# Kernel tuning notes

Measured on AMD Instinct MI355X. Metric: run time of the kernel, lower is better.

## Reference

```python
import jax, jax.numpy as jnp
import numpy as np

# ---- module hyperparameters (from init_kwargs) ----
K_CURV = 1.0      # Lorentz curvature k
MAX_NORM = 1000.0 # rescale_to_max cap on space-norm (assumed)
KSIZE = 5
STRIDE = 2
PAD = 2
IN_CH = 257       # includes time dim -> 256 space channels
OUT_CH = 257
LIN_FEATS = (IN_CH - 1) * KSIZE + 1  # 1281
EPS = 1e-8


def _add_time(space):
    # time = sqrt(k + ||space||^2), concat on last axis
    time = jnp.sqrt(K_CURV + jnp.sum(space * space, axis=-1, keepdims=True))
    return jnp.concatenate([time, space], axis=-1)


def _rescale_to_max(x):
    # clamp space-norm to MAX_NORM, then recompute valid time component
    space = x[..., 1:]
    norm = jnp.sqrt(jnp.sum(space * space, axis=-1, keepdims=True))
    scale = jnp.minimum(1.0, MAX_NORM / jnp.maximum(norm, EPS))
    return _add_time(space * scale)


def setup_inputs() -> dict:
    key = jax.random.key(0)
    kx, kw, kb = jax.random.split(key, 3)
    x = jax.random.normal(kx, (16, 8192, IN_CH), dtype=jnp.float32)
    W = jax.random.normal(kw, (OUT_CH, LIN_FEATS), dtype=jnp.float32) * 0.02
    b = jax.random.normal(kb, (OUT_CH,), dtype=jnp.float32) * 0.01
    return {"x": x, "W": W, "b": b}


def reference(x, W, b):
    B, L, C = x.shape
    # pad length dim with zeros (time channel of padded frames is clamped in
    # torch, but the time channel is discarded before add_time, so only the
    # space channels matter)
    xp = jnp.pad(x, ((0, 0), (PAD, PAD), (0, 0)))
    space = xp[..., 1:]                                  # (B, Lp, C-1)
    Lp = L + 2 * PAD
    n_frames = (Lp - KSIZE) // STRIDE + 1
    # im2col gather: (n_frames, K) window indices
    idx = jnp.arange(n_frames)[:, None] * STRIDE + jnp.arange(KSIZE)[None, :]
    patches = space[:, idx, :]                           # (B, n, K, C-1)
    # torch reorders to kernel-major (k, c) layout before add_time
    ps = patches.reshape(B, n_frames, KSIZE * (C - 1))   # (B, n, K*(C-1))
    pk = _add_time(ps)                                   # (B, n, lin_feats)
    out = jnp.einsum('bnf,of->bno', pk, W) + b           # LorentzProjection
    out = _add_time(out[..., 1:])                        # manifold.projx
    out = _rescale_to_max(out)                           # rescale_after=True
    return out
```

## Files before the change

### kernel.cpp

```cpp
#include <hip/hip_runtime.h>
#include <hip/hip_bf16.h>
#include <cstdint>
#include <cstddef>

namespace {

constexpr int BATCH = 16;
constexpr int LEN   = 8192;
constexpr int CIN   = 257;
constexpr int CS    = 256;
constexpr int NF    = 4096;
constexpr int KG    = 1280;
constexpr int MT    = 128;
constexpr int NITER = 20;

constexpr size_t WT_BYTES = (size_t)CS * KG * 2;
constexpr size_t W0_OFF   = WT_BYTES;
constexpr size_t WS_NEED  = W0_OFF + (size_t)CS * 4;

typedef __attribute__((ext_vector_type(8))) short short8;
typedef __attribute__((ext_vector_type(8))) unsigned short ushort8v;
typedef __attribute__((ext_vector_type(4))) float f32x4;

__device__ __forceinline__ unsigned short f2bf_bits(float f) {
  union { __hip_bfloat16 h; unsigned short u; } cv;
  cv.h = __float2bfloat16(f);
  return cv.u;
}

__device__ __forceinline__ void async_cp16(const void* g, void* l) {
  __builtin_amdgcn_global_load_lds(
      (const __attribute__((address_space(1))) void*)g,
      (__attribute__((address_space(3))) void*)l,
      16, 0, 0);
}

}

__global__ void prep_w_kernel(const float* __restrict__ W,
                              __hip_bfloat16* __restrict__ wt,
                              float* __restrict__ w0) {
  int n = blockIdx.x;
  const float* wrow = W + (size_t)(n + 1) * 1281;
  for (int k = threadIdx.x; k < KG; k += blockDim.x)
    wt[(size_t)n * KG + k] = __float2bfloat16(wrow[1 + k]);
  if (threadIdx.x == 0) w0[n] = wrow[0];
}

__global__ __launch_bounds__(512, 2) void lorentz_fused_kernel(
    const float* __restrict__ x,
    const __hip_bfloat16* __restrict__ wt,
    const float* __restrict__ w0,
    const float* __restrict__ bvec,
    float* __restrict__ out) {
  __shared__ alignas(16) char lds[98304];
  __shared__ alignas(16) float time0_s[128];
  __shared__ alignas(16) float normsq_s[128];
  char* const A0 = lds;
  char* const A1 = lds + 16384;
  char* const B0 = lds + 32768;
  char* const B1 = lds + 65536;

  const int tid   = threadIdx.x;
  const int w     = tid >> 6;
  const int lane  = tid & 63;
  const int row16 = lane & 15;
  const int q     = lane >> 4;
  const int mh    = w >> 2;
  const int nq    = w & 3;
  const int lg    = lane >> 3;
  const int lc    = lane & 7;
  const int csw   = lc ^ lg;

  const int bx    = blockIdx.x;
  const int b     = bx >> 5;
  const int Mblk  = (bx & 31) * MT;

  const int m0 = w * 16 + lg;
  const int m1 = m0 + 8;
  const float* xb = x + (size_t)b * LEN * CIN;

  f32x4 acc[4][4];
#pragma unroll
  for (int i = 0; i < 4; ++i)
#pragma unroll
    for (int j = 0; j < 4; ++j) acc[i][j] = (f32x4){0.f, 0.f, 0.f, 0.f};

  float ssq0 = 0.f, ssq1 = 0.f;
  f32x4 a00, a01, a10, a11;

  auto loadA = [&](int it) {
    const int kk = it >> 2;
    const int c0 = (it & 3) << 6;
    const int coff = 1 + c0 + lc * 8;
    const int t0 = 2 * (Mblk + m0) + kk - 2;
    const int t1 = t0 + 16;
    a00 = (f32x4){0.f, 0.f, 0.f, 0.f};
    a01 = a00; a10 = a00; a11 = a00;
    if ((unsigned)t0 < (unsigned)LEN) {
      const float* g = xb + (size_t)t0 * CIN + coff;
      __builtin_memcpy(&a00, g, 16);
      __builtin_memcpy(&a01, g + 4, 16);
    }
    if ((unsigned)t1 < (unsigned)LEN) {
      const float* g = xb + (size_t)t1 * CIN + coff;
      __builtin_memcpy(&a10, g, 16);
      __builtin_memcpy(&a11, g + 4, 16);
    }
  };

  auto writeA = [&](char* A) {
    ssq0 += a00[0]*a00[0] + a00[1]*a00[1] + a00[2]*a00[2] + a00[3]*a00[3]
          + a01[0]*a01[0] + a01[1]*a01[1] + a01[2]*a01[2] + a01[3]*a01[3];
    ssq1 += a10[0]*a10[0] + a10[1]*a10[1] + a10[2]*a10[2] + a10[3]*a10[3]
          + a11[0]*a11[0] + a11[1]*a11[1] + a11[2]*a11[2] + a11[3]*a11[3];
    ushort8v u0, u1;
#pragma unroll
    for (int i = 0; i < 4; ++i) {
      u0[i]     = f2bf_bits(a00[i]);
      u0[4 + i] = f2bf_bits(a01[i]);
      u1[i]     = f2bf_bits(a10[i]);
      u1[4 + i] = f2bf_bits(a11[i]);
    }
    *(ushort8v*)(A + ((m0 * 8 + csw) << 4)) = u0;
    *(ushort8v*)(A + ((m1 * 8 + csw) << 4)) = u1;
  };

  auto stageB = [&](int it, char* B) {
    const int k0 = it << 6;
#pragma unroll
    for (int j = 0; j < 4; ++j) {
      const int n = w * 32 + j * 8 + lg;
      async_cp16(wt + (size_t)n * KG + k0 + csw * 8, B + (w * 4 + j) * 1024);
    }
  };

  auto compute = [&](const char* A, const char* B) {
#pragma unroll
    for (int s = 0; s < 2; ++s) {
      const int p = (s * 4 + q) ^ lc;
      short8 bfr[4];
#pragma unroll
      for (int nt = 0; nt < 4; ++nt)
        bfr[nt] = *(const short8*)(B + (((nq * 64 + nt * 16 + row16) * 8 + p) << 4));
#pragma unroll
      for (int mt = 0; mt < 4; ++mt) {
        short8 af = *(const short8*)(A + (((mh * 64 + mt * 16 + row16) * 8 + p) << 4));
#pragma unroll
        for (int nt = 0; nt < 4; ++nt)
          acc[mt][nt] = __builtin_amdgcn_mfma_f32_16x16x32_bf16(
              af, bfr[nt], acc[mt][nt], 0, 0, 0);
      }
    }
  };

  loadA(0);
  stageB(0, B0);
  asm volatile("s_waitcnt vmcnt(4)" ::: "memory");
  writeA(A0);
  loadA(1);
  asm volatile("s_waitcnt lgkmcnt(0)" ::: "memory");

  for (int it = 0; it < NITER; ++it) {
    char* Ac = (it & 1) ? A1 : A0;
    char* Bc = (it & 1) ? B1 : B0;
    if (it < NITER - 1) {
      char* An = (it & 1) ? A0 : A1;
      char* Bn = (it & 1) ? B0 : B1;
      stageB(it + 1, Bn);
      asm volatile("s_waitcnt vmcnt(4)" ::: "memory");
      writeA(An);
      if (it < NITER - 2) loadA(it + 2);
    } else {
      asm volatile("s_waitcnt vmcnt(0)" ::: "memory");
    }
    asm volatile("" ::: "memory");
    __builtin_amdgcn_s_barrier();
    asm volatile("" ::: "memory");
    compute(Ac, Bc);
    asm volatile("" ::: "memory");
    __builtin_amdgcn_s_barrier();
    asm volatile("" ::: "memory");
  }

  if (tid < 128) normsq_s[tid] = 0.0f;
  {
    float s0 = ssq0;
    s0 += __shfl_xor(s0, 1); s0 += __shfl_xor(s0, 2); s0 += __shfl_xor(s0, 4);
    float s1 = ssq1;
    s1 += __shfl_xor(s1, 1); s1 += __shfl_xor(s1, 2); s1 += __shfl_xor(s1, 4);
    if (lc == 0) {
      time0_s[m0] = sqrtf(1.0f + s0);
      time0_s[m1] = sqrtf(1.0f + s1);
    }
  }
  __syncthreads();

  float w0v[4], bv[4];
#pragma unroll
  for (int nt = 0; nt < 4; ++nt) {
    int n = nq * 64 + nt * 16 + row16;
    w0v[nt] = w0[n];
    bv[nt]  = bvec[1 + n];
  }

#pragma unroll
  for (int mt = 0; mt < 4; ++mt) {
    f32x4 t4 = *(const f32x4*)&time0_s[mh * 64 + mt * 16 + q * 4];
#pragma unroll
    for (int nt = 0; nt < 4; ++nt)
#pragma unroll
      for (int r = 0; r < 4; ++r)
        acc[mt][nt][r] = acc[mt][nt][r] + t4[r] * w0v[nt] + bv[nt];
#pragma unroll
    for (int r = 0; r < 4; ++r) {
      float ps = 0.f;
#pragma unroll
      for (int nt = 0; nt < 4; ++nt) ps += acc[mt][nt][r] * acc[mt][nt][r];
      ps += __shfl_xor(ps, 1);
      ps += __shfl_xor(ps, 2);
      ps += __shfl_xor(ps, 4);
      ps += __shfl_xor(ps, 8);
      if (row16 == 0) atomicAdd(&normsq_s[mh * 64 + mt * 16 + q * 4 + r], ps);
    }
  }
  __syncthreads();

#pragma unroll
  for (int mt = 0; mt < 4; ++mt) {
#pragma unroll
    for (int r = 0; r < 4; ++r) {
      int m = mh * 64 + mt * 16 + q * 4 + r;
      float nsq  = normsq_s[m];
      float norm = sqrtf(nsq);
      float scale = fminf(1.0f, 1000.0f / fmaxf(norm, 1e-8f));
      size_t ob = ((size_t)b * NF + Mblk + m) * 257;
#pragma unroll
      for (int nt = 0; nt < 4; ++nt) {
        int n = nq * 64 + nt * 16 + row16;
        out[ob + 1 + n] = acc[mt][nt][r] * scale;
      }
    }
  }
  if (tid < 128) {
    float nsq  = normsq_s[tid];
    float norm = sqrtf(nsq);
    float scale = fminf(1.0f, 1000.0f / fmaxf(norm, 1e-8f));
    size_t ob = ((size_t)b * NF + Mblk + tid) * 257;
    out[ob] = sqrtf(1.0f + scale * scale * nsq);
  }
}

__global__ void fallback_kernel(const float* __restrict__ x,
                                const float* __restrict__ W,
                                const float* __restrict__ bvec,
                                float* __restrict__ out) {
  int fid = blockIdx.x;
  int b = fid >> 12;
  int g = fid & (NF - 1);
  __shared__ float patch[1280];
  __shared__ float red[256];
  int tid = threadIdx.x;
  float ss = 0.f;
  for (int k = tid; k < 1280; k += 256) {
    int kk = k >> 8, c = k & 255;
    int t = 2 * g + kk - 2;
    float v = (t >= 0 && t < LEN) ? x[((size_t)b * LEN + t) * CIN + 1 + c] : 0.f;
    patch[k] = v;
    ss += v * v;
  }
  red[tid] = ss;
  __syncthreads();
  for (int off = 128; off > 0; off >>= 1) {
    if (tid < off) red[tid] += red[tid + off];
    __syncthreads();
  }
  float time0 = sqrtf(1.f + red[0]);
  __syncthreads();
  const float* wrow = W + (size_t)(tid + 1) * 1281;
  float acc = time0 * wrow[0] + bvec[tid + 1];
  for (int k = 0; k < 1280; ++k) acc += wrow[1 + k] * patch[k];
  red[tid] = acc * acc;
  __syncthreads();
  for (int off = 128; off > 0; off >>= 1) {
    if (tid < off) red[tid] += red[tid + off];
    __syncthreads();
  }
  float nsq = red[0];
  float norm = sqrtf(nsq);
  float scale = fminf(1.f, 1000.f / fmaxf(norm, 1e-8f));
  size_t ob = ((size_t)b * NF + g) * 257;
  out[ob + 1 + tid] = acc * scale;
  if (tid == 0) out[ob] = sqrtf(1.f + scale * scale * nsq);
}

extern "C" void kernel_launch(void* const* d_in, const int* in_sizes, int n_in,
                              void* d_out, int out_size, void* d_ws, size_t ws_size,
                              hipStream_t stream) {
  const float* x  = (const float*)d_in[0];
  const float* W  = (const float*)d_in[1];
  const float* bv = (const float*)d_in[2];
  float* out = (float*)d_out;

  if (ws_size >= WS_NEED) {
    char* ws = (char*)d_ws;
    __hip_bfloat16* wt = (__hip_bfloat16*)ws;
    float* w0          = (float*)(ws + W0_OFF);
    prep_w_kernel<<<256, 256, 0, stream>>>(W, wt, w0);
    lorentz_fused_kernel<<<BATCH * (NF / MT), 512, 0, stream>>>(x, wt, w0, bv, out);
  } else {
    fallback_kernel<<<BATCH * NF, 256, 0, stream>>>(x, W, bv, out);
  }
}
```

Measured before the change: 268.8 us.

## Replace double-buffered LDS pipeline with single buffer to halve shared memory

Drops the ping-pong A/B LDS buffers in favour of one 48KB buffer set. Each iteration now writes A, issues the async B copy, prefetches the next A tile and then computes, with two full __syncthreads per iteration. The aim is to let two 512-thread blocks reside per CU instead of one, so the 512-block grid can run in a single wave. The cost is the in-block overlap of loads with MFMA compute: the barriers likely force outstanding global loads to drain before compute.

```diff
diff --git a/kernel.cpp b/kernel.cpp
--- a/kernel.cpp
+++ b/kernel.cpp
@@ -53,13 +53,10 @@
     const float* __restrict__ w0,
     const float* __restrict__ bvec,
     float* __restrict__ out) {
-  __shared__ alignas(16) char lds[98304];
+  __shared__ alignas(16) char A_lds[16384];
+  __shared__ alignas(16) char B_lds[32768];
   __shared__ alignas(16) float time0_s[128];
   __shared__ alignas(16) float normsq_s[128];
-  char* const A0 = lds;
-  char* const A1 = lds + 16384;
-  char* const B0 = lds + 32768;
-  char* const B1 = lds + 65536;
 
   const int tid   = threadIdx.x;
   const int w     = tid >> 6;
@@ -109,7 +106,7 @@
     }
   };
 
-  auto writeA = [&](char* A) {
+  auto writeA = [&]() {
     ssq0 += a00[0]*a00[0] + a00[1]*a00[1] + a00[2]*a00[2] + a00[3]*a00[3]
           + a01[0]*a01[0] + a01[1]*a01[1] + a01[2]*a01[2] + a01[3]*a01[3];
     ssq1 += a10[0]*a10[0] + a10[1]*a10[1] + a10[2]*a10[2] + a10[3]*a10[3]
@@ -122,30 +119,30 @@
       u1[i]     = f2bf_bits(a10[i]);
       u1[4 + i] = f2bf_bits(a11[i]);
     }
-    *(ushort8v*)(A + ((m0 * 8 + csw) << 4)) = u0;
-    *(ushort8v*)(A + ((m1 * 8 + csw) << 4)) = u1;
-  };
-
-  auto stageB = [&](int it, char* B) {
+    *(ushort8v*)(A_lds + ((m0 * 8 + csw) << 4)) = u0;
+    *(ushort8v*)(A_lds + ((m1 * 8 + csw) << 4)) = u1;
+  };
+
+  auto stageB = [&](int it) {
     const int k0 = it << 6;
 #pragma unroll
     for (int j = 0; j < 4; ++j) {
       const int n = w * 32 + j * 8 + lg;
-      async_cp16(wt + (size_t)n * KG + k0 + csw * 8, B + (w * 4 + j) * 1024);
-    }
-  };
-
-  auto compute = [&](const char* A, const char* B) {
+      async_cp16(wt + (size_t)n * KG + k0 + csw * 8, B_lds + (w * 4 + j) * 1024);
+    }
+  };
+
+  auto compute = [&]() {
 #pragma unroll
     for (int s = 0; s < 2; ++s) {
       const int p = (s * 4 + q) ^ lc;
       short8 bfr[4];
 #pragma unroll
       for (int nt = 0; nt < 4; ++nt)
-        bfr[nt] = *(const short8*)(B + (((nq * 64 + nt * 16 + row16) * 8 + p) << 4));
+        bfr[nt] = *(const short8*)(B_lds + (((nq * 64 + nt * 16 + row16) * 8 + p) << 4));
 #pragma unroll
       for (int mt = 0; mt < 4; ++mt) {
-        short8 af = *(const short8*)(A + (((mh * 64 + mt * 16 + row16) * 8 + p) << 4));
+        short8 af = *(const short8*)(A_lds + (((mh * 64 + mt * 16 + row16) * 8 + p) << 4));
 #pragma unroll
         for (int nt = 0; nt < 4; ++nt)
           acc[mt][nt] = __builtin_amdgcn_mfma_f32_16x16x32_bf16(
@@ -155,34 +152,16 @@
   };
 
   loadA(0);
-  stageB(0, B0);
-  asm volatile("s_waitcnt vmcnt(4)" ::: "memory");
-  writeA(A0);
-  loadA(1);
-  asm volatile("s_waitcnt lgkmcnt(0)" ::: "memory");
-
   for (int it = 0; it < NITER; ++it) {
-    char* Ac = (it & 1) ? A1 : A0;
-    char* Bc = (it & 1) ? B1 : B0;
-    if (it < NITER - 1) {
-      char* An = (it & 1) ? A0 : A1;
-      char* Bn = (it & 1) ? B0 : B1;
-      stageB(it + 1, Bn);
-      asm volatile("s_waitcnt vmcnt(4)" ::: "memory");
-      writeA(An);
-      if (it < NITER - 2) loadA(it + 2);
-    } else {
-      asm volatile("s_waitcnt vmcnt(0)" ::: "memory");
-    }
-    asm volatile("" ::: "memory");
-    __builtin_amdgcn_s_barrier();
-    asm volatile("" ::: "memory");
-    compute(Ac, Bc);
-    asm volatile("" ::: "memory");
-    __builtin_amdgcn_s_barrier();
-    asm volatile("" ::: "memory");
-  }
-
+    __syncthreads();
+    writeA();
+    stageB(it);
+    if (it + 1 < NITER) loadA(it + 1);
+    __syncthreads();
+    compute();
+  }
+
+  __syncthreads();
   if (tid < 128) normsq_s[tid] = 0.0f;
   {
     float s0 = ssq0;
```

Result: slower. 285.5 us (+6.2%).

## Triple-buffer B tiles and overlap A staging with split MFMA phases

Applied to the files above, without the earlier changes.

Restructures the main loop into a deeper software pipeline. B tiles go into three LDS buffers and are prefetched two iterations ahead. A tiles use two alternating register sets, and the bf16 conversion and LDS write of the next A tile sit between the two k-halves of the MFMA work. The loop now needs one barrier per iteration instead of two, and s_setprio raises wave priority around the MFMA bursts. The cost is more LDS (an extra 32 KB B buffer), more live registers, and vmcnt bookkeeping that depends on the exact count of outstanding loads.

```diff
diff --git a/kernel.cpp b/kernel.cpp
--- a/kernel.cpp
+++ b/kernel.cpp
@@ -22,6 +22,8 @@
 typedef __attribute__((ext_vector_type(8))) unsigned short ushort8v;
 typedef __attribute__((ext_vector_type(4))) float f32x4;
 
+struct ARegs { f32x4 a00, a01, a10, a11; };
+
 __device__ __forceinline__ unsigned short f2bf_bits(float f) {
   union { __hip_bfloat16 h; unsigned short u; } cv;
   cv.h = __float2bfloat16(f);
@@ -53,13 +55,10 @@
     const float* __restrict__ w0,
     const float* __restrict__ bvec,
     float* __restrict__ out) {
-  __shared__ alignas(16) char lds[98304];
+  __shared__ alignas(16) char Ab[2][16384];
+  __shared__ alignas(16) char Bb[3][32768];
   __shared__ alignas(16) float time0_s[128];
   __shared__ alignas(16) float normsq_s[128];
-  char* const A0 = lds;
-  char* const A1 = lds + 16384;
-  char* const B0 = lds + 32768;
-  char* const B1 = lds + 65536;
 
   const int tid   = threadIdx.x;
   const int w     = tid >> 6;
@@ -86,41 +85,41 @@
 #pragma unroll
     for (int j = 0; j < 4; ++j) acc[i][j] = (f32x4){0.f, 0.f, 0.f, 0.f};
 
+  ARegs afE, afO;
   float ssq0 = 0.f, ssq1 = 0.f;
-  f32x4 a00, a01, a10, a11;
-
-  auto loadA = [&](int it) {
+
+  auto loadA = [&](int it, ARegs& af) {
     const int kk = it >> 2;
     const int c0 = (it & 3) << 6;
     const int coff = 1 + c0 + lc * 8;
     const int t0 = 2 * (Mblk + m0) + kk - 2;
     const int t1 = t0 + 16;
-    a00 = (f32x4){0.f, 0.f, 0.f, 0.f};
-    a01 = a00; a10 = a00; a11 = a00;
+    af.a00 = (f32x4){0.f, 0.f, 0.f, 0.f};
+    af.a01 = af.a00; af.a10 = af.a00; af.a11 = af.a00;
     if ((unsigned)t0 < (unsigned)LEN) {
       const float* g = xb + (size_t)t0 * CIN + coff;
-      __builtin_memcpy(&a00, g, 16);
-      __builtin_memcpy(&a01, g + 4, 16);
+      __builtin_memcpy(&af.a00, g, 16);
+      __builtin_memcpy(&af.a01, g + 4, 16);
     }
     if ((unsigned)t1 < (unsigned)LEN) {
       const float* g = xb + (size_t)t1 * CIN + coff;
-      __builtin_memcpy(&a10, g, 16);
-      __builtin_memcpy(&a11, g + 4, 16);
-    }
-  };
-
-  auto writeA = [&](char* A) {
-    ssq0 += a00[0]*a00[0] + a00[1]*a00[1] + a00[2]*a00[2] + a00[3]*a00[3]
-          + a01[0]*a01[0] + a01[1]*a01[1] + a01[2]*a01[2] + a01[3]*a01[3];
-    ssq1 += a10[0]*a10[0] + a10[1]*a10[1] + a10[2]*a10[2] + a10[3]*a10[3]
-          + a11[0]*a11[0] + a11[1]*a11[1] + a11[2]*a11[2] + a11[3]*a11[3];
+      __builtin_memcpy(&af.a10, g, 16);
+      __builtin_memcpy(&af.a11, g + 4, 16);
+    }
+  };
+
+  auto writeA = [&](char* A, ARegs& af) {
+    ssq0 += af.a00[0]*af.a00[0] + af.a00[1]*af.a00[1] + af.a00[2]*af.a00[2] + af.a00[3]*af.a00[3]
+          + af.a01[0]*af.a01[0] + af.a01[1]*af.a01[1] + af.a01[2]*af.a01[2] + af.a01[3]*af.a01[3];
+    ssq1 += af.a10[0]*af.a10[0] + af.a10[1]*af.a10[1] + af.a10[2]*af.a10[2] + af.a10[3]*af.a10[3]
+          + af.a11[0]*af.a11[0] + af.a11[1]*af.a11[1] + af.a11[2]*af.a11[2] + af.a11[3]*af.a11[3];
     ushort8v u0, u1;
 #pragma unroll
     for (int i = 0; i < 4; ++i) {
-      u0[i]     = f2bf_bits(a00[i]);
-      u0[4 + i] = f2bf_bits(a01[i]);
-      u1[i]     = f2bf_bits(a10[i]);
-      u1[4 + i] = f2bf_bits(a11[i]);
+      u0[i]     = f2bf_bits(af.a00[i]);
+      u0[4 + i] = f2bf_bits(af.a01[i]);
+      u1[i]     = f2bf_bits(af.a10[i]);
+      u1[4 + i] = f2bf_bits(af.a11[i]);
     }
     *(ushort8v*)(A + ((m0 * 8 + csw) << 4)) = u0;
     *(ushort8v*)(A + ((m1 * 8 + csw) << 4)) = u1;
@@ -135,54 +134,63 @@
     }
   };
 
-  auto compute = [&](const char* A, const char* B) {
-#pragma unroll
-    for (int s = 0; s < 2; ++s) {
-      const int p = (s * 4 + q) ^ lc;
-      short8 bfr[4];
+  auto mfma_s = [&](const char* A, const char* B, int s) {
+    const int p = (s * 4 + q) ^ lc;
+    short8 bfr[4];
+#pragma unroll
+    for (int nt = 0; nt < 4; ++nt)
+      bfr[nt] = *(const short8*)(B + (((nq * 64 + nt * 16 + row16) * 8 + p) << 4));
+    __builtin_amdgcn_s_setprio(1);
+#pragma unroll
+    for (int mt = 0; mt < 4; ++mt) {
+      short8 af = *(const short8*)(A + (((mh * 64 + mt * 16 + row16) * 8 + p) << 4));
 #pragma unroll
       for (int nt = 0; nt < 4; ++nt)
-        bfr[nt] = *(const short8*)(B + (((nq * 64 + nt * 16 + row16) * 8 + p) << 4));
-#pragma unroll
-      for (int mt = 0; mt < 4; ++mt) {
-        short8 af = *(const short8*)(A + (((mh * 64 + mt * 16 + row16) * 8 + p) << 4));
-#pragma unroll
-        for (int nt = 0; nt < 4; ++nt)
-          acc[mt][nt] = __builtin_amdgcn_mfma_f32_16x16x32_bf16(
-              af, bfr[nt], acc[mt][nt], 0, 0, 0);
-      }
-    }
-  };
-
-  loadA(0);
-  stageB(0, B0);
-  asm volatile("s_waitcnt vmcnt(4)" ::: "memory");
-  writeA(A0);
-  loadA(1);
+        acc[mt][nt] = __builtin_amdgcn_mfma_f32_16x16x32_bf16(
+            af, bfr[nt], acc[mt][nt], 0, 0, 0);
+    }
+    __builtin_amdgcn_s_setprio(0);
+  };
+
+  stageB(0, Bb[0]);
+  loadA(0, afE);
+  asm volatile("s_waitcnt vmcnt(0)" ::: "memory");
+  writeA(Ab[0], afE);
+  loadA(1, afO);
+  stageB(1, Bb[1]);
   asm volatile("s_waitcnt lgkmcnt(0)" ::: "memory");
-
-  for (int it = 0; it < NITER; ++it) {
-    char* Ac = (it & 1) ? A1 : A0;
-    char* Bc = (it & 1) ? B1 : B0;
-    if (it < NITER - 1) {
-      char* An = (it & 1) ? A0 : A1;
-      char* Bn = (it & 1) ? B0 : B1;
-      stageB(it + 1, Bn);
+  asm volatile("" ::: "memory");
+  __builtin_amdgcn_s_barrier();
+  asm volatile("" ::: "memory");
+
+  auto iterBody = [&](int it, ARegs& regsC, ARegs& regsF) {
+    char* Acur = Ab[it & 1];
+    char* Anxt = Ab[(it + 1) & 1];
+    char* Bcur = Bb[it % 3];
+    if (it + 2 < NITER) stageB(it + 2, Bb[(it + 2) % 3]);
+    mfma_s(Acur, Bcur, 0);
+    if (it + 2 < NITER) {
       asm volatile("s_waitcnt vmcnt(4)" ::: "memory");
-      writeA(An);
-      if (it < NITER - 2) loadA(it + 2);
-    } else {
+    } else if (it + 1 < NITER) {
       asm volatile("s_waitcnt vmcnt(0)" ::: "memory");
     }
-    asm volatile("" ::: "memory");
-    __builtin_amdgcn_s_barrier();
-    asm volatile("" ::: "memory");
-    compute(Ac, Bc);
-    asm volatile("" ::: "memory");
-    __builtin_amdgcn_s_barrier();
-    asm volatile("" ::: "memory");
-  }
-
+    if (it + 1 < NITER) writeA(Anxt, regsC);
+    if (it + 2 < NITER) loadA(it + 2, regsF);
+    mfma_s(Acur, Bcur, 1);
+    if (it + 1 < NITER) {
+      asm volatile("s_waitcnt lgkmcnt(0)" ::: "memory");
+      asm volatile("" ::: "memory");
+      __builtin_amdgcn_s_barrier();
+      asm volatile("" ::: "memory");
+    }
+  };
+
+  for (int it = 0; it < NITER; it += 2) {
+    iterBody(it,     afO, afE);
+    iterBody(it + 1, afE, afO);
+  }
+
+  __syncthreads();
   if (tid < 128) normsq_s[tid] = 0.0f;
   {
     float s0 = ssq0;
```

Result: slower. 277.1 us (+3.1%).

## Pre-convert x to padded bf16 and use 256-row GEMM tiles with async loads

Applied to the files above, without the earlier changes.

Adds a prep pass that converts x to a padded bf16 buffer and precomputes per-row squared norms. A new GEMM kernel then streams A and B tiles straight into LDS with async global-to-LDS copies, uses 256x256 output tiles with triple-buffered B, and raises MFMA priority. The intent is to halve the activation bytes the GEMM reads and to cut per-block conversion and reduction work, at the cost of an extra full pass over x and a large workspace. With 160KB of LDS per block, occupancy drops to one block per CU.

```diff
diff --git a/kernel.cpp b/kernel.cpp
--- a/kernel.cpp
+++ b/kernel.cpp
@@ -11,12 +11,18 @@
 constexpr int CS    = 256;
 constexpr int NF    = 4096;
 constexpr int KG    = 1280;
-constexpr int MT    = 128;
 constexpr int NITER = 20;
-
-constexpr size_t WT_BYTES = (size_t)CS * KG * 2;
-constexpr size_t W0_OFF   = WT_BYTES;
-constexpr size_t WS_NEED  = W0_OFF + (size_t)CS * 4;
+constexpr int LPAD  = LEN + 4;
+
+constexpr size_t XS_BYTES  = (size_t)BATCH * LPAD * CS * 2;
+constexpr size_t RSQ_OFF   = XS_BYTES;
+constexpr size_t RSQ_BYTES = (size_t)BATCH * LPAD * 4;
+constexpr size_t WT1_OFF   = RSQ_OFF + RSQ_BYTES;
+constexpr size_t W01_OFF   = WT1_OFF + (size_t)CS * KG * 2;
+constexpr size_t WS1_NEED  = W01_OFF + (size_t)CS * 4;
+
+constexpr size_t W02_OFF  = (size_t)CS * KG * 2;
+constexpr size_t WS2_NEED = W02_OFF + (size_t)CS * 4;
 
 typedef __attribute__((ext_vector_type(8))) short short8;
 typedef __attribute__((ext_vector_type(8))) unsigned short ushort8v;
@@ -47,19 +53,254 @@
   if (threadIdx.x == 0) w0[n] = wrow[0];
 }
 
+__global__ void prep_x_kernel(const float* __restrict__ x,
+                              __hip_bfloat16* __restrict__ xs,
+                              float* __restrict__ rowsq) {
+  const int tid = threadIdx.x;
+  const int bx  = blockIdx.x;
+  if (bx < 8192) {
+    __shared__ float4 xf4[1028];
+    const float4* src = (const float4*)(x + (size_t)bx * 4112);
+#pragma unroll
+    for (int i = 0; i < 4; ++i) {
+      int idx = i * 256 + tid;
+      xf4[idx] = src[idx];
+    }
+    if (tid < 4) xf4[1024 + tid] = src[1024 + tid];
+    __syncthreads();
+    const float* xf = (const float*)xf4;
+    const int row = tid >> 4, seg = tid & 15;
+    const float* v = xf + row * 257 + 1 + seg * 16;
+    float ss = 0.f;
+    unsigned short u[16];
+#pragma unroll
+    for (int i = 0; i < 16; ++i) {
+      float f = v[i];
+      ss += f * f;
+      u[i] = f2bf_bits(f);
+    }
+    const int b = bx >> 9;
+    const int t = (bx & 511) * 16 + row;
+    const size_t tpg = (size_t)b * LPAD + 2 + t;
+    ushort8v* dst = (ushort8v*)((unsigned short*)xs + tpg * CS + seg * 16);
+    ushort8v p0, p1;
+#pragma unroll
+    for (int i = 0; i < 8; ++i) { p0[i] = u[i]; p1[i] = u[8 + i]; }
+    dst[0] = p0;
+    dst[1] = p1;
+    ss += __shfl_xor(ss, 1);
+    ss += __shfl_xor(ss, 2);
+    ss += __shfl_xor(ss, 4);
+    ss += __shfl_xor(ss, 8);
+    if (seg == 0) rowsq[tpg] = ss;
+  } else {
+    for (int i = tid; i < 64 * 128; i += 256) {
+      int row = i >> 7, uo = i & 127;
+      int b = row >> 2, j = row & 3;
+      size_t tpg = (size_t)b * LPAD + (j < 2 ? j : 8192 + j);
+      ((uint32_t*)xs)[tpg * 128 + uo] = 0;
+      if (uo == 0) rowsq[tpg] = 0.0f;
+    }
+  }
+}
+
+__global__ __launch_bounds__(512, 2) void lorentz_gemm8_kernel(
+    const __hip_bfloat16* __restrict__ xs,
+    const __hip_bfloat16* __restrict__ wt,
+    const float* __restrict__ rowsq,
+    const float* __restrict__ w0,
+    const float* __restrict__ bvec,
+    float* __restrict__ out) {
+  __shared__ alignas(16) char lds[163840];
+
+  const int tid   = threadIdx.x;
+  const int w     = tid >> 6;
+  const int lane  = tid & 63;
+  const int row16 = lane & 15;
+  const int q     = lane >> 4;
+  const int wr    = w >> 2;
+  const int wc    = w & 3;
+  const int lg    = lane >> 3;
+  const int lc    = lane & 7;
+  const int csw   = lc ^ lg;
+
+  const int bx    = blockIdx.x;
+  const int b     = bx >> 4;
+  const int Mblk  = (bx & 15) * 256;
+
+  const __hip_bfloat16* xsb = xs + (size_t)b * LPAD * CS;
+
+  f32x4 acc[8][4];
+#pragma unroll
+  for (int i = 0; i < 8; ++i)
+#pragma unroll
+    for (int j = 0; j < 4; ++j) acc[i][j] = (f32x4){0.f, 0.f, 0.f, 0.f};
+
+  auto stgA = [&](int t, int hf, char* buf) {
+    char* dst = buf + hf * 16384 + w * 2048;
+#pragma unroll
+    for (int j = 0; j < 2; ++j) {
+      const int r  = w * 16 + j * 8 + lg;
+      const int rp = 2 * (Mblk + hf * 128 + r) + (t >> 2);
+      async_cp16(xsb + (size_t)rp * CS + ((t & 3) << 6) + csw * 8,
+                 dst + j * 1024);
+    }
+  };
+  auto stgB = [&](int t, int hf, char* buf) {
+    char* dst = buf + hf * 16384 + w * 2048;
+#pragma unroll
+    for (int j = 0; j < 2; ++j) {
+      const int n = hf * 128 + w * 16 + j * 8 + lg;
+      async_cp16(wt + (size_t)n * KG + (t << 6) + csw * 8, dst + j * 1024);
+    }
+  };
+
+  auto rdA = [&](const char* Ah, int mt, int s) -> short8 {
+    const int lr = mt * 16 + row16;
+    const int p  = (s * 4 + q) ^ lc;
+    return *(const short8*)(Ah + ((lr * 8 + p) << 4));
+  };
+  auto rdB = [&](const char* Bh, int nt, int s) -> short8 {
+    const int lr = (wc & 1) * 64 + nt * 16 + row16;
+    const int p  = (s * 4 + q) ^ lc;
+    return *(const short8*)(Bh + ((lr * 8 + p) << 4));
+  };
+
+  char* Acur = lds;
+  char* Aalt = lds + 32768;
+  char* Bcur = lds + 65536;
+  char* Bnx  = lds + 65536 + 32768;
+  char* Bnn  = lds + 65536 + 65536;
+
+  stgB(0, 0, Bcur); stgB(0, 1, Bcur);
+  stgA(0, 0, Acur); stgA(0, 1, Acur);
+  stgB(1, 0, Bnx);  stgB(1, 1, Bnx);
+  asm volatile("s_waitcnt vmcnt(4)" ::: "memory");
+  asm volatile("" ::: "memory");
+  __builtin_amdgcn_s_barrier();
+  asm volatile("" ::: "memory");
+
+  for (int t = 0; t < NITER; ++t) {
+    const char* Ah = Acur + (wr << 14);
+    const char* Bh = Bcur + ((wc >> 1) << 14);
+    short8 bfr[4];
+#pragma unroll
+    for (int p = 0; p < 4; ++p) {
+      const int s  = p >> 1;
+      const int mb = (p & 1) << 2;
+      short8 afr[4];
+      if ((p & 1) == 0) {
+#pragma unroll
+        for (int nt = 0; nt < 4; ++nt) bfr[nt] = rdB(Bh, nt, s);
+      }
+#pragma unroll
+      for (int i = 0; i < 4; ++i) afr[i] = rdA(Ah, mb + i, s);
+      if (p == 0 && t + 1 < NITER) stgA(t + 1, 0, Aalt);
+      if (p == 1 && t + 1 < NITER) stgA(t + 1, 1, Aalt);
+      if (p == 2 && t + 2 < NITER) stgB(t + 2, 0, Bnn);
+      if (p == 3 && t + 2 < NITER) stgB(t + 2, 1, Bnn);
+      asm volatile("" ::: "memory");
+      __builtin_amdgcn_s_barrier();
+      asm volatile("s_waitcnt lgkmcnt(0)" ::: "memory");
+      __builtin_amdgcn_sched_barrier(0);
+      __builtin_amdgcn_s_setprio(1);
+#pragma unroll
+      for (int i = 0; i < 4; ++i)
+#pragma unroll
+        for (int nt = 0; nt < 4; ++nt)
+          acc[mb + i][nt] = __builtin_amdgcn_mfma_f32_16x16x32_bf16(
+              afr[i], bfr[nt], acc[mb + i][nt], 0, 0, 0);
+      __builtin_amdgcn_s_setprio(0);
+      __builtin_amdgcn_sched_barrier(0);
+      if (p == 3) {
+        if (t + 2 < NITER) { asm volatile("s_waitcnt vmcnt(4)" ::: "memory"); }
+        else               { asm volatile("s_waitcnt vmcnt(0)" ::: "memory"); }
+      }
+      asm volatile("" ::: "memory");
+      __builtin_amdgcn_s_barrier();
+      asm volatile("" ::: "memory");
+    }
+    char* tA = Acur; Acur = Aalt; Aalt = tA;
+    char* tB = Bcur; Bcur = Bnx; Bnx = Bnn; Bnn = tB;
+  }
+
+  __syncthreads();
+  float* time0_s  = (float*)lds;
+  float* normsq_s = (float*)(lds + 1024);
+  if (tid < 256) {
+    const float* rs = rowsq + (size_t)b * LPAD + 2 * (Mblk + tid);
+    float s5 = rs[0] + rs[1] + rs[2] + rs[3] + rs[4];
+    time0_s[tid]  = sqrtf(1.0f + s5);
+    normsq_s[tid] = 0.0f;
+  }
+  __syncthreads();
+
+  float w0v[4], bv[4];
+#pragma unroll
+  for (int nt = 0; nt < 4; ++nt) {
+    int n = wc * 64 + nt * 16 + row16;
+    w0v[nt] = w0[n];
+    bv[nt]  = bvec[1 + n];
+  }
+
+#pragma unroll
+  for (int mt = 0; mt < 8; ++mt) {
+    f32x4 t4 = *(const f32x4*)&time0_s[wr * 128 + mt * 16 + q * 4];
+#pragma unroll
+    for (int nt = 0; nt < 4; ++nt)
+#pragma unroll
+      for (int r = 0; r < 4; ++r)
+        acc[mt][nt][r] = acc[mt][nt][r] + t4[r] * w0v[nt] + bv[nt];
+#pragma unroll
+    for (int r = 0; r < 4; ++r) {
+      float ps = 0.f;
+#pragma unroll
+      for (int nt = 0; nt < 4; ++nt) ps += acc[mt][nt][r] * acc[mt][nt][r];
+      ps += __shfl_xor(ps, 1);
+      ps += __shfl_xor(ps, 2);
+      ps += __shfl_xor(ps, 4);
+      ps += __shfl_xor(ps, 8);
+      if (row16 == 0)
+        atomicAdd(&normsq_s[wr * 128 + mt * 16 + q * 4 + r], ps);
+    }
+  }
+  __syncthreads();
+
+#pragma unroll
+  for (int mt = 0; mt < 8; ++mt) {
+#pragma unroll
+    for (int r = 0; r < 4; ++r) {
+      int m = wr * 128 + mt * 16 + q * 4 + r;
+      float nsq  = normsq_s[m];
+      float norm = sqrtf(nsq);
+      float scale = fminf(1.0f, 1000.0f / fmaxf(norm, 1e-8f));
+      size_t ob = ((size_t)b * NF + Mblk + m) * 257;
+#pragma unroll
+      for (int nt = 0; nt < 4; ++nt) {
+        int n = wc * 64 + nt * 16 + row16;
+        out[ob + 1 + n] = acc[mt][nt][r] * scale;
+      }
+    }
+  }
+  if (tid < 256) {
+    float nsq  = normsq_s[tid];
+    float norm = sqrtf(nsq);
+    float scale = fminf(1.0f, 1000.0f / fmaxf(norm, 1e-8f));
+    size_t ob = ((size_t)b * NF + Mblk + tid) * 257;
+    out[ob] = sqrtf(1.0f + scale * scale * nsq);
+  }
+}
+
 __global__ __launch_bounds__(512, 2) void lorentz_fused_kernel(
     const float* __restrict__ x,
     const __hip_bfloat16* __restrict__ wt,
     const float* __restrict__ w0,
     const float* __restrict__ bvec,
     float* __restrict__ out) {
-  __shared__ alignas(16) char lds[98304];
+  __shared__ alignas(16) char ldsA[2][16384];
+  __shared__ alignas(16) char ldsB[2][32768];
   __shared__ alignas(16) float time0_s[128];
   __shared__ alignas(16) float normsq_s[128];
-  char* const A0 = lds;
-  char* const A1 = lds + 16384;
-  char* const B0 = lds + 32768;
-  char* const B1 = lds + 65536;
 
   const int tid   = threadIdx.x;
   const int w     = tid >> 6;
@@ -74,7 +315,7 @@
 
   const int bx    = blockIdx.x;
   const int b     = bx >> 5;
-  const int Mblk  = (bx & 31) * MT;
+  const int Mblk  = (bx & 31) * 128;
 
   const int m0 = w * 16 + lg;
   const int m1 = m0 + 8;
@@ -155,18 +396,18 @@
   };
 
   loadA(0);
-  stageB(0, B0);
+  stageB(0, ldsB[0]);
   asm volatile("s_waitcnt vmcnt(4)" ::: "memory");
-  writeA(A0);
+  writeA(ldsA[0]);
   loadA(1);
   asm volatile("s_waitcnt lgkmcnt(0)" ::: "memory");
 
   for (int it = 0; it < NITER; ++it) {
-    char* Ac = (it & 1) ? A1 : A0;
-    char* Bc = (it & 1) ? B1 : B0;
+    char* Ac = ldsA[it & 1];
+    char* Bc = ldsB[it & 1];
     if (it < NITER - 1) {
-      char* An = (it & 1) ? A0 : A1;
-      char* Bn = (it & 1) ? B0 : B1;
+      char* An = ldsA[(it + 1) & 1];
+      char* Bn = ldsB[(it + 1) & 1];
       stageB(it + 1, Bn);
       asm volatile("s_waitcnt vmcnt(4)" ::: "memory");
       writeA(An);
@@ -183,6 +424,7 @@
     asm volatile("" ::: "memory");
   }
 
+  __syncthreads();
   if (tid < 128) normsq_s[tid] = 0.0f;
   {
     float s0 = ssq0;
@@ -301,13 +543,23 @@
   const float* W  = (const float*)d_in[1];
   const float* bv = (const float*)d_in[2];
   float* out = (float*)d_out;
-
-  if (ws_size >= WS_NEED) {
-    char* ws = (char*)d_ws;
+  char* ws = (char*)d_ws;
+
+  if (ws_size >= WS1_NEED) {
+    __hip_bfloat16* xs = (__hip_bfloat16*)ws;
+    float* rowsq       = (float*)(ws + RSQ_OFF);
+    __hip_bfloat16* wt = (__hip_bfloat16*)(ws + WT1_OFF);
+    float* w0          = (float*)(ws + W01_OFF);
+    prep_w_kernel<<<256, 256, 0, stream>>>(W, wt, w0);
+    prep_x_kernel<<<8193, 256, 0, stream>>>(x, xs, rowsq);
+    lorentz_gemm8_kernel<<<BATCH * (NF / 256), 512, 0, stream>>>(
+        xs, wt, rowsq, w0, bv, out);
+  } else if (ws_size >= WS2_NEED) {
     __hip_bfloat16* wt = (__hip_bfloat16*)ws;
-    float* w0          = (float*)(ws + W0_OFF);
+    float* w0          = (float*)(ws + W02_OFF);
     prep_w_kernel<<<256, 256, 0, stream>>>(W, wt, w0);
-    lorentz_fused_kernel<<<BATCH * (NF / MT), 512, 0, stream>>>(x, wt, w0, bv, out);
+    lorentz_fused_kernel<<<BATCH * (NF / 128), 512, 0, stream>>>(
+        x, wt, w0, bv, out);
   } else {
     fallback_kernel<<<BATCH * NF, 256, 0, stream>>>(x, W, bv, out);
   }
```

Result: slower. 279.0 us (+3.8%).
